# Performance work log

Measured on AMD Instinct MI355X. Metric: run time of the kernel, lower is better.

The kernel has to match this reference:

```python
import jax, jax.numpy as jnp
import numpy as np


def setup_inputs() -> dict:
    key = jax.random.key(0)
    k1, k2 = jax.random.split(key)
    B, M, L, C, F, K = 8, 32, 1024, 256, 256, 3
    x = jax.random.normal(k1, (B, M, L, C), dtype=jnp.float32)
    W = jax.random.normal(k2, (K, C, F), dtype=jnp.float32) * 0.02  # WIO layout
    b = jnp.zeros((F,), dtype=jnp.float32)
    return {"x": x, "W": W, "b": b}


def reference(x, W, b):
    # Original: tf.map_fn(Conv1D, x) over leading axis of [B, M, L, C].
    # Mathematically identical to one batched 'valid' Conv1D on [B*M, L, C].
    B, M, L, C = x.shape
    K, _, F = W.shape
    xf = x.reshape(B * M, L, C)
    y = jax.lax.conv_general_dilated(
        xf, W,
        window_strides=(1,),
        padding='VALID',
        dimension_numbers=('NWC', 'WIO', 'NWC'),
    ) + b
    return y.reshape(B, M, L - K + 1, F)
```

## Files before the change

### kernel.cpp

```cpp
#include <hip/hip_runtime.h>

typedef __attribute__((ext_vector_type(8))) short short8;
typedef __attribute__((ext_vector_type(4))) float f32x4;

constexpr int L = 1024, C = 256, F = 256;
constexpr int NIMG = 256;
constexpr int LOUT = 1022;
constexpr long MAXROW = (long)NIMG * L - 1;

__device__ inline unsigned short f2bf(float f) {
  union { float f; unsigned u; } v; v.f = f;
  return (unsigned short)((v.u + 0x7FFFu + ((v.u >> 16) & 1u)) >> 16);
}

__device__ inline void g2l16(const unsigned short* g, unsigned short* l) {
  __builtin_amdgcn_global_load_lds(
      (const __attribute__((address_space(1))) unsigned int*)g,
      (__attribute__((address_space(3))) unsigned int*)l, 16, 0, 0);
}

__global__ void wprep(const float* __restrict__ W, unsigned short* __restrict__ Wt) {
  int tid = blockIdx.x * 256 + threadIdx.x;
  int kc = tid >> 8, f = tid & 255;
  int k = kc >> 8, c = kc & 255;
  int slab = c >> 5, kp = c & 31;
  Wt[(size_t)(((slab * 3 + k) * 256 + f) * 32 + kp)] = f2bf(W[tid]);
}

__global__ __launch_bounds__(512, 2) void conv_mfma(
    const float* __restrict__ x, const unsigned short* __restrict__ Wt,
    const float* __restrict__ bias, float* __restrict__ y)
{
  __shared__ __align__(16) unsigned short As[2][1032 * 8];
  __shared__ __align__(16) unsigned short Bs[3][512 * 16];

  const int bid = blockIdx.x;
  const int mt  = bid & 3;
  const int img = bid >> 2;
  const int l0  = mt * 256;

  const int tid  = threadIdx.x;
  const int lane = tid & 63;
  const int wv   = tid >> 6;
  const int wr   = wv >> 2;
  const int wc   = wv & 3;
  const int lr   = lane & 15;
  const int quad = lane >> 4;

  f32x4 acc[8][4] = {};
  float4 av[2][2];
  float4 avt[2];

  const long gb = (long)img * L + l0;

  auto issue_A = [&](int slab) {
    const int cb = slab * 32;
    long g0 = gb + (tid >> 2);        if (g0 > MAXROW) g0 = MAXROW;
    long g1 = gb + 128 + (tid >> 2);  if (g1 > MAXROW) g1 = MAXROW;
    const float* p0 = x + g0 * C + cb + (tid & 3) * 8;
    const float* p1 = x + g1 * C + cb + (tid & 3) * 8;
    av[0][0] = *(const float4*)p0; av[0][1] = *(const float4*)(p0 + 4);
    av[1][0] = *(const float4*)p1; av[1][1] = *(const float4*)(p1 + 4);
    if (tid < 8) {
      long g2 = gb + 256 + (tid >> 2); if (g2 > MAXROW) g2 = MAXROW;
      const float* p2 = x + g2 * C + cb + (tid & 3) * 8;
      avt[0] = *(const float4*)p2; avt[1] = *(const float4*)(p2 + 4);
    }
  };

  auto pack8 = [&](float4 a, float4 b) {
    short8 r;
    r[0] = (short)f2bf(a.x); r[1] = (short)f2bf(a.y);
    r[2] = (short)f2bf(a.z); r[3] = (short)f2bf(a.w);
    r[4] = (short)f2bf(b.x); r[5] = (short)f2bf(b.y);
    r[6] = (short)f2bf(b.z); r[7] = (short)f2bf(b.w);
    return r;
  };

  auto write_A = [&](int ab2) {
    *(short8*)(As[ab2] + (size_t)tid * 8)         = pack8(av[0][0], av[0][1]);
    *(short8*)(As[ab2] + (size_t)(tid + 512) * 8) = pack8(av[1][0], av[1][1]);
    if (tid < 8)
      *(short8*)(As[ab2] + (size_t)(1024 + tid) * 8) = pack8(avt[0], avt[1]);
  };

  auto stage_B = [&](int tile, int bb) {
    const unsigned short* bsrc = Wt + (size_t)tile * 8192;
    g2l16(bsrc + (size_t)tid * 8,         Bs[bb] + (size_t)tid * 8);
    g2l16(bsrc + (size_t)(tid + 512) * 8, Bs[bb] + (size_t)(tid + 512) * 8);
  };

  issue_A(0);
  stage_B(0, 0);
  stage_B(1, 1);
  write_A(0);

  for (int slab = 0; slab < 8; ++slab) {
    const int ab = slab & 1;
#pragma unroll
    for (int k = 0; k < 3; ++k) {
      if (slab < 7) {
        if (k == 0)      asm volatile("s_waitcnt vmcnt(2) lgkmcnt(0)" ::: "memory");
        else             asm volatile("s_waitcnt vmcnt(6)" ::: "memory");
      } else {
        if (k == 0)      asm volatile("s_waitcnt vmcnt(2) lgkmcnt(0)" ::: "memory");
        else if (k == 1) asm volatile("s_waitcnt vmcnt(2)" ::: "memory");
        else             asm volatile("s_waitcnt vmcnt(0)" ::: "memory");
      }
      __builtin_amdgcn_s_barrier();
      __builtin_amdgcn_sched_barrier(0);

      const int t = slab * 3 + k;
      if (t < 22) stage_B(t + 2, (k + 2) % 3);
      if (k == 0 && slab < 7) issue_A(slab + 1);

      short8 af[8], bf[4];
#pragma unroll
      for (int mi = 0; mi < 8; ++mi)
        af[mi] = *(const short8*)(As[ab] + (wr * 128 + mi * 16 + lr + k) * 32 + quad * 8);
#pragma unroll
      for (int ni = 0; ni < 4; ++ni)
        bf[ni] = *(const short8*)(Bs[k] + (wc * 64 + ni * 16 + lr) * 32 + quad * 8);

      __builtin_amdgcn_s_setprio(1);
#pragma unroll
      for (int mi = 0; mi < 8; ++mi)
#pragma unroll
        for (int ni = 0; ni < 4; ++ni)
          acc[mi][ni] = __builtin_amdgcn_mfma_f32_16x16x32_bf16(af[mi], bf[ni], acc[mi][ni], 0, 0, 0);
      __builtin_amdgcn_s_setprio(0);

      if (k == 2 && slab < 7) write_A(ab ^ 1);
    }
  }

  float bv[4];
#pragma unroll
  for (int ni = 0; ni < 4; ++ni)
    bv[ni] = bias[wc * 64 + ni * 16 + lr];

#pragma unroll
  for (int mi = 0; mi < 8; ++mi) {
#pragma unroll
    for (int r = 0; r < 4; ++r) {
      const int lrow = l0 + wr * 128 + mi * 16 + quad * 4 + r;
      if (lrow < LOUT) {
        float* yp = y + ((size_t)img * LOUT + lrow) * F + wc * 64 + lr;
#pragma unroll
        for (int ni = 0; ni < 4; ++ni)
          yp[ni * 16] = acc[mi][ni][r] + bv[ni];
      }
    }
  }
}

extern "C" void kernel_launch(void* const* d_in, const int* in_sizes, int n_in,
                              void* d_out, int out_size, void* d_ws, size_t ws_size,
                              hipStream_t stream) {
  const float* x = (const float*)d_in[0];
  const float* W = (const float*)d_in[1];
  const float* b = (const float*)d_in[2];
  float* y = (float*)d_out;
  unsigned short* Wt = (unsigned short*)d_ws;

  wprep<<<768, 256, 0, stream>>>(W, Wt);
  conv_mfma<<<NIMG * 4, 512, 0, stream>>>(x, Wt, b, y);
}
```

Baseline: 478.5 us.

## Split each tap into two MFMA halves with extra barriers and interleaved LDS reads

Restructures the per-tap inner loop so each wave loads only half its A fragments at a time. It runs the first 16 MFMAs, then reads the second half of A, and writes the next slab's A, between the two MFMA halves. Explicit barriers and lgkmcnt waits are added around each half, and the vmcnt counts are retuned for the new ordering. The aim is to cut register pressure and interleave LDS traffic with matrix work, at the cost of more block-wide barriers per tap.

```diff
diff --git a/kernel.cpp b/kernel.cpp
--- a/kernel.cpp
+++ b/kernel.cpp
@@ -35,9 +35,9 @@
   __shared__ __align__(16) unsigned short Bs[3][512 * 16];
 
   const int bid = blockIdx.x;
-  const int mt  = bid & 3;
+  const int lt  = bid & 3;
   const int img = bid >> 2;
-  const int l0  = mt * 256;
+  const int l0  = lt * 256;
 
   const int tid  = threadIdx.x;
   const int lane = tid & 63;
@@ -77,11 +77,11 @@
     return r;
   };
 
-  auto write_A = [&](int ab2) {
-    *(short8*)(As[ab2] + (size_t)tid * 8)         = pack8(av[0][0], av[0][1]);
-    *(short8*)(As[ab2] + (size_t)(tid + 512) * 8) = pack8(av[1][0], av[1][1]);
+  auto write_A = [&](int p) {
+    *(short8*)(As[p] + (size_t)tid * 8)         = pack8(av[0][0], av[0][1]);
+    *(short8*)(As[p] + (size_t)(tid + 512) * 8) = pack8(av[1][0], av[1][1]);
     if (tid < 8)
-      *(short8*)(As[ab2] + (size_t)(1024 + tid) * 8) = pack8(avt[0], avt[1]);
+      *(short8*)(As[p] + (size_t)(1024 + tid) * 8) = pack8(avt[0], avt[1]);
   };
 
   auto stage_B = [&](int tile, int bb) {
@@ -90,49 +90,63 @@
     g2l16(bsrc + (size_t)(tid + 512) * 8, Bs[bb] + (size_t)(tid + 512) * 8);
   };
 
-  issue_A(0);
+  auto read_af = [&](int p, int k, int mi) {
+    return *(const short8*)(As[p] + (size_t)((wr * 128 + mi * 16 + lr + k) * 4 + quad) * 8);
+  };
+  auto read_bf = [&](int buf, int ni) {
+    return *(const short8*)(Bs[buf] + (size_t)((wc * 64 + ni * 16 + lr) * 4 + quad) * 8);
+  };
+
+#define BAR   __builtin_amdgcn_s_barrier()
+#define SBAR  __builtin_amdgcn_sched_barrier(0)
+#define LGKM0 asm volatile("s_waitcnt lgkmcnt(0)" ::: "memory")
+#define MFMA_HALF(H)                                                          \
+  do {                                                                        \
+    __builtin_amdgcn_s_setprio(1);                                            \
+    _Pragma("unroll")                                                         \
+    for (int mi = 0; mi < 4; ++mi)                                            \
+      _Pragma("unroll")                                                       \
+      for (int ni = 0; ni < 4; ++ni)                                          \
+        acc[(H) * 4 + mi][ni] = __builtin_amdgcn_mfma_f32_16x16x32_bf16(      \
+            af[mi], bf[ni], acc[(H) * 4 + mi][ni], 0, 0, 0);                  \
+    __builtin_amdgcn_s_setprio(0);                                            \
+  } while (0)
+
+#define TAP(S, TAU, VM, STG, DOA, DOWA)                                       \
+  do {                                                                        \
+    asm volatile("s_waitcnt vmcnt(" #VM ")" ::: "memory");                    \
+    BAR; SBAR;                                                                \
+    short8 af[4], bf[4];                                                      \
+    if ((STG) >= 0) stage_B((STG), ((TAU) + 2) % 3);                          \
+    if (DOA) issue_A((S) + 1);                                                \
+    _Pragma("unroll")                                                         \
+    for (int mi = 0; mi < 4; ++mi) af[mi] = read_af((S) & 1, (TAU), mi);      \
+    _Pragma("unroll")                                                         \
+    for (int ni = 0; ni < 4; ++ni) bf[ni] = read_bf((TAU), ni);               \
+    SBAR; BAR; LGKM0; SBAR;                                                   \
+    MFMA_HALF(0);                                                             \
+    BAR;                                                                      \
+    _Pragma("unroll")                                                         \
+    for (int mi = 0; mi < 4; ++mi) af[mi] = read_af((S) & 1, (TAU), 4 + mi);  \
+    if (DOWA) write_A(((S) & 1) ^ 1);                                         \
+    SBAR; BAR; LGKM0; SBAR;                                                   \
+    MFMA_HALF(1);                                                             \
+  } while (0)
+
   stage_B(0, 0);
   stage_B(1, 1);
+  issue_A(0);
   write_A(0);
+  LGKM0;
 
-  for (int slab = 0; slab < 8; ++slab) {
-    const int ab = slab & 1;
-#pragma unroll
-    for (int k = 0; k < 3; ++k) {
-      if (slab < 7) {
-        if (k == 0)      asm volatile("s_waitcnt vmcnt(2) lgkmcnt(0)" ::: "memory");
-        else             asm volatile("s_waitcnt vmcnt(6)" ::: "memory");
-      } else {
-        if (k == 0)      asm volatile("s_waitcnt vmcnt(2) lgkmcnt(0)" ::: "memory");
-        else if (k == 1) asm volatile("s_waitcnt vmcnt(2)" ::: "memory");
-        else             asm volatile("s_waitcnt vmcnt(0)" ::: "memory");
-      }
-      __builtin_amdgcn_s_barrier();
-      __builtin_amdgcn_sched_barrier(0);
-
-      const int t = slab * 3 + k;
-      if (t < 22) stage_B(t + 2, (k + 2) % 3);
-      if (k == 0 && slab < 7) issue_A(slab + 1);
-
-      short8 af[8], bf[4];
-#pragma unroll
-      for (int mi = 0; mi < 8; ++mi)
-        af[mi] = *(const short8*)(As[ab] + (wr * 128 + mi * 16 + lr + k) * 32 + quad * 8);
-#pragma unroll
-      for (int ni = 0; ni < 4; ++ni)
-        bf[ni] = *(const short8*)(Bs[k] + (wc * 64 + ni * 16 + lr) * 32 + quad * 8);
-
-      __builtin_amdgcn_s_setprio(1);
-#pragma unroll
-      for (int mi = 0; mi < 8; ++mi)
-#pragma unroll
-        for (int ni = 0; ni < 4; ++ni)
-          acc[mi][ni] = __builtin_amdgcn_mfma_f32_16x16x32_bf16(af[mi], bf[ni], acc[mi][ni], 0, 0, 0);
-      __builtin_amdgcn_s_setprio(0);
-
-      if (k == 2 && slab < 7) write_A(ab ^ 1);
-    }
+  for (int s = 0; s < 7; ++s) {
+    TAP(s, 0, 2, 3 * s + 2, 1, 0);
+    TAP(s, 1, 4, 3 * s + 3, 0, 0);
+    TAP(s, 2, 4, 3 * s + 4, 0, 1);
   }
+  TAP(7, 0, 2, 23, 0, 0);
+  TAP(7, 1, 2, -1, 0, 0);
+  TAP(7, 2, 0, -1, 0, 0);
 
   float bv[4];
 #pragma unroll
@@ -152,6 +166,11 @@
       }
     }
   }
+#undef TAP
+#undef MFMA_HALF
+#undef BAR
+#undef SBAR
+#undef LGKM0
 }
 
 extern "C" void kernel_launch(void* const* d_in, const int* in_sizes, int n_in,
```

After: 490.5 us. 1.03x slower.
